# Performance work log

Hardware: AMD Instinct MI355X
Metric: run time of the kernel (lower is better)

## Reference

```python
import jax, jax.numpy as jnp
import numpy as np

HEADS = 8
DIM_HEAD = 64


def setup_inputs() -> dict:
    key = jax.random.key(0)
    ks = jax.random.split(key, 4)
    dim, h, w = 256, 64, 64
    hidden = HEADS * DIM_HEAD  # 512
    return {
        "x": jax.random.normal(ks[0], (dim, h, w), dtype=jnp.float32),
        "gamma": jnp.zeros((dim, 1, 1), dtype=jnp.float32),
        "mem_kv": jax.random.normal(ks[1], (2, HEADS, 4, DIM_HEAD), dtype=jnp.float32),
        "w_qkv": jax.random.normal(ks[2], (3 * hidden, dim), dtype=jnp.float32) * (dim ** -0.5),
        "w_out": jax.random.normal(ks[3], (dim, hidden), dtype=jnp.float32) * (hidden ** -0.5),
    }


def reference(x, gamma, mem_kv, w_qkv, w_out):
    c, h, w = x.shape
    scale = DIM_HEAD ** -0.5
    # RMSNorm over channel axis (axis 0), computed in fp32 like precision_cast
    xf = x.astype(jnp.float32)
    xn = (xf / jnp.linalg.norm(xf, ord=2, axis=0) * (gamma + 1.0) * (c ** 0.5)).astype(x.dtype)
    # 1x1 conv == channel matmul: (3*hidden, c) @ (c, h*w)
    qkv = jnp.einsum('oc,chw->ohw', w_qkv, xn)
    q, k, v = jnp.split(qkv, 3, axis=0)
    # '(h c) x y -> h (x y) c' with heads outermost in the channel dim
    def to_tokens(t):
        return t.reshape(HEADS, DIM_HEAD, h * w).transpose(0, 2, 1)  # [H, S, D]
    q, k, v = map(to_tokens, (q, k, v))
    k = jnp.concatenate([mem_kv[0], k], axis=-2)  # [H, M+S, D]
    v = jnp.concatenate([mem_kv[1], v], axis=-2)
    sim = jnp.einsum('hid,hjd->hij', q * scale, k)  # [H, S, M+S]
    # softmax(sim - global_max) in fp32 == stable softmax along last axis
    attn = jax.nn.softmax((sim - jnp.max(sim)).astype(jnp.float32), axis=-1).astype(sim.dtype)
    out = jnp.einsum('hij,hjd->hid', attn, v)  # [H, S, D]
    # 'h (x y) d -> (h d) x y'
    out = out.reshape(HEADS, h, w, DIM_HEAD).transpose(0, 3, 1, 2).reshape(HEADS * DIM_HEAD, h, w)
    return jnp.einsum('oc,chw->ohw', w_out, out)
```

## Files before the change

kernel.cpp:

```cpp
#include <hip/hip_runtime.h>
#include <hip/hip_bf16.h>
#include <math.h>

#define C_DIM 256
#define SPAT 4096
#define HEADS_N 8
#define DHEAD 64
#define MEMTOK 4
#define TTOK 4100
#define TTOKP 4160
#define HID 512
#define PSP 72

typedef __bf16 bf16x8 __attribute__((ext_vector_type(8)));
typedef unsigned short u16x8 __attribute__((ext_vector_type(8)));
typedef float f32x4 __attribute__((ext_vector_type(4)));

static __device__ inline unsigned short f2bf(float f) {
    unsigned int u = __float_as_uint(f);
    u += 0x7fffu + ((u >> 16) & 1u);
    return (unsigned short)(u >> 16);
}

static __device__ inline bf16x8 ldb8(const unsigned short* p) {
    union { u16x8 u; bf16x8 b; } t;
    t.u = *(const u16x8*)p;
    return t.b;
}

static __device__ inline unsigned int pkbf(float a, float b) {
    union { __bf16 h[2]; unsigned int u; } t;
    t.h[0] = (__bf16)a; t.h[1] = (__bf16)b;
    return t.u;
}

static __device__ inline void gload16(const void* g, void* l) {
    __builtin_amdgcn_global_load_lds(
        (const __attribute__((address_space(1))) unsigned int*)g,
        (__attribute__((address_space(3))) unsigned int*)l, 16, 0, 0);
}

__global__ __launch_bounds__(256) void prep_kernel(
    const float* __restrict__ x, const float* __restrict__ gamma,
    const float* __restrict__ mem, const float* __restrict__ wq,
    const float* __restrict__ wo,
    unsigned short* __restrict__ xb, float* __restrict__ spb,
    unsigned short* __restrict__ wb, unsigned short* __restrict__ wob,
    unsigned short* __restrict__ kb, unsigned short* __restrict__ vtb) {
    __shared__ float XT[64][65];
    __shared__ float red[4][64];
    const int bid = blockIdx.x;
    const int t = threadIdx.x;
    if (bid < 256) {
        int p0 = (bid & 63) * 64, c0 = (bid >> 6) * 64;
#pragma unroll
        for (int i = 0; i < 4; ++i) {
            int cl = i * 16 + (t >> 4), p4 = (t & 15) * 4;
            *(float4*)&XT[cl][p4] = *(const float4*)&x[(size_t)(c0 + cl) * SPAT + p0 + p4];
        }
        __syncthreads();
        int pl = t >> 2, cs = (t & 3) * 16;
        u16x8 a, b;
#pragma unroll
        for (int j = 0; j < 8; ++j) a[j] = f2bf(XT[cs + j][pl]);
#pragma unroll
        for (int j = 0; j < 8; ++j) b[j] = f2bf(XT[cs + 8 + j][pl]);
        *(u16x8*)&xb[(size_t)(p0 + pl) * C_DIM + c0 + cs] = a;
        *(u16x8*)&xb[(size_t)(p0 + pl) * C_DIM + c0 + cs + 8] = b;
    } else if (bid < 320) {
        int p = (bid - 256) * 64 + (t & 63);
        int g = t >> 6;
        float ss = 0.f;
        for (int c = g * 64; c < g * 64 + 64; ++c) {
            float v = x[(size_t)c * SPAT + p];
            ss += v * v;
        }
        red[g][t & 63] = ss;
        __syncthreads();
        if (g == 0) {
            int lp = t & 63;
            float tot = red[0][lp] + red[1][lp] + red[2][lp] + red[3][lp];
            spb[p] = rsqrtf(tot) * 16.0f;
        }
    } else if (bid < 512) {
        size_t idx = ((size_t)(bid - 320) * 256 + t) * 8;
        int c0 = (int)(idx & 255);
        float4 f0 = *(const float4*)&wq[idx];
        float4 f1 = *(const float4*)&wq[idx + 4];
        float4 g0 = *(const float4*)&gamma[c0];
        float4 g1 = *(const float4*)&gamma[c0 + 4];
        u16x8 pk;
        pk[0] = f2bf(f0.x * (g0.x + 1.f)); pk[1] = f2bf(f0.y * (g0.y + 1.f));
        pk[2] = f2bf(f0.z * (g0.z + 1.f)); pk[3] = f2bf(f0.w * (g0.w + 1.f));
        pk[4] = f2bf(f1.x * (g1.x + 1.f)); pk[5] = f2bf(f1.y * (g1.y + 1.f));
        pk[6] = f2bf(f1.z * (g1.z + 1.f)); pk[7] = f2bf(f1.w * (g1.w + 1.f));
        *(u16x8*)&wb[idx] = pk;
    } else if (bid < 576) {
        size_t idx = ((size_t)(bid - 512) * 256 + t) * 8;
        float4 f0 = *(const float4*)&wo[idx];
        float4 f1 = *(const float4*)&wo[idx + 4];
        u16x8 pk;
        pk[0] = f2bf(f0.x); pk[1] = f2bf(f0.y); pk[2] = f2bf(f0.z); pk[3] = f2bf(f0.w);
        pk[4] = f2bf(f1.x); pk[5] = f2bf(f1.y); pk[6] = f2bf(f1.z); pk[7] = f2bf(f1.w);
        *(u16x8*)&wob[idx] = pk;
    } else {
        int i = (bid - 576) * 256 + t;
        if (i < 4096) {
            int d = i & 63, m = (i >> 6) & 3, h = (i >> 8) & 7, s = (i >> 11) & 1;
            unsigned short val = f2bf(mem[i]);
            if (s == 0) kb[(size_t)h * TTOKP * 64 + m * 64 + d] = val;
            else        vtb[((size_t)h * 64 + d) * TTOKP + m] = val;
        } else {
            int z = i - 4096;
            if (z < 30720) {
                int h = z / 3840, r = z % 3840;
                int row = TTOK + r / 64, d = r % 64;
                kb[(size_t)h * TTOKP * 64 + row * 64 + d] = 0;
            } else {
                z -= 30720;
                int h = z / 3840, r = z % 3840;
                int d = r / 60, tcol = TTOK + r % 60;
                vtb[((size_t)h * 64 + d) * TTOKP + tcol] = 0;
            }
        }
    }
}

__global__ __launch_bounds__(256) void qkv_mfma(const unsigned short* __restrict__ wb,
                                                const unsigned short* __restrict__ xb,
                                                const float* __restrict__ spb,
                                                unsigned short* __restrict__ qb,
                                                unsigned short* __restrict__ kb,
                                                unsigned short* __restrict__ vtb) {
    const int tile_p = blockIdx.x;
    const int tile_o = blockIdx.y;
    const int p0 = tile_p * 64, o0 = tile_o * 64;
    __shared__ unsigned short SW[64 * 256];
    __shared__ unsigned short SX[64 * 256];

    const int t = threadIdx.x;
    const int w = t >> 6, lane = t & 63;
    const int col16 = lane & 15, quad = lane >> 4;

    {
        const char* gw = (const char*)(wb + (size_t)o0 * C_DIM);
        const char* gx = (const char*)(xb + (size_t)p0 * C_DIM);
#pragma unroll
        for (int i = 0; i < 8; ++i) {
            int chunk = i * 4 + w;
            int row = chunk * 2 + (lane >> 5);
            int b = (lane & 31) * 16;
            int src = row * 512 + (b ^ ((row & 7) << 4));
            gload16(gw + src, (char*)SW + chunk * 1024);
            gload16(gx + src, (char*)SX + chunk * 1024);
        }
    }
    asm volatile("s_waitcnt vmcnt(0)\n\ts_barrier" ::: "memory");
    __builtin_amdgcn_sched_barrier(0);

    const int cs = (col16 & 7) << 4;
    const char* swp = (const char*)SW;
    const char* sxp = (const char*)SX;
    const int arow = (w * 16 + col16) * 512;
    f32x4 acc[4];
#pragma unroll
    for (int n = 0; n < 4; ++n) acc[n] = (f32x4){0.f, 0.f, 0.f, 0.f};
#pragma unroll
    for (int kk = 0; kk < 8; ++kk) {
        int ko = (kk * 64 + quad * 16) ^ cs;
        bf16x8 a = ldb8((const unsigned short*)(swp + arow + ko));
#pragma unroll
        for (int n = 0; n < 4; ++n) {
            bf16x8 b = ldb8((const unsigned short*)(sxp + (n * 16 + col16) * 512 + ko));
            acc[n] = __builtin_amdgcn_mfma_f32_16x16x32_bf16(a, b, acc[n], 0, 0, 0);
        }
    }

    float spv[4];
#pragma unroll
    for (int n = 0; n < 4; ++n) spv[n] = spb[p0 + n * 16 + col16];

    const int sec = tile_o >> 3, h = tile_o & 7;
    if (sec < 2) {
        const float qsc = (sec == 0) ? 0.125f * 1.4426950408889634f : 1.0f;
        unsigned short* Ot = SW;
        __syncthreads();
#pragma unroll
        for (int n = 0; n < 4; ++n) {
            float s = qsc * spv[n];
            ushort4 v4 = {f2bf(acc[n][0] * s), f2bf(acc[n][1] * s),
                          f2bf(acc[n][2] * s), f2bf(acc[n][3] * s)};
            *(ushort4*)&Ot[(n * 16 + col16) * PSP + w * 16 + quad * 4] = v4;
        }
        __syncthreads();
        int prow = t >> 2, dseg = t & 3;
        u16x8 va = *(u16x8*)&Ot[prow * PSP + dseg * 16];
        u16x8 vb = *(u16x8*)&Ot[prow * PSP + dseg * 16 + 8];
        unsigned short* dst = (sec == 0)
            ? qb + (size_t)h * SPAT * 64 + (size_t)(p0 + prow) * 64
            : kb + (size_t)h * TTOKP * 64 + (size_t)(MEMTOK + p0 + prow) * 64;
        *(u16x8*)&dst[dseg * 16] = va;
        *(u16x8*)&dst[dseg * 16 + 8] = vb;
    } else {
        unsigned short* dst = vtb + (size_t)h * 64 * TTOKP;
#pragma unroll
        for (int n = 0; n < 4; ++n) {
            int tcol = MEMTOK + p0 + n * 16 + col16;
            float s = spv[n];
#pragma unroll
            for (int r = 0; r < 4; ++r)
                dst[(size_t)(w * 16 + quad * 4 + r) * TTOKP + tcol] = f2bf(acc[n][r] * s);
        }
    }
}

__global__ __launch_bounds__(256) void attn_mfma(const unsigned short* __restrict__ qb,
                                                 const unsigned short* __restrict__ kb,
                                                 const unsigned short* __restrict__ vtb,
                                                 unsigned short* __restrict__ obb) {
    const int h  = blockIdx.x & 7;
    const int p0 = (blockIdx.x >> 3) * 64;

    __shared__ unsigned short Ks0[64 * 64], Ks1[64 * 64];
    __shared__ unsigned short Vs0[64 * 64], Vs1[64 * 64];
    __shared__ __bf16 Psb[4 * 16 * PSP];

    const int t = threadIdx.x;
    const int w = t >> 6;
    const int lane = t & 63;
    const int col16 = lane & 15;
    const int quad = lane >> 4;

    const unsigned short* qh = qb + (size_t)h * SPAT * 64;
    const char* khb = (const char*)(kb + (size_t)h * TTOKP * 64);
    const char* vhb = (const char*)(vtb + (size_t)h * 64 * TTOKP);

    const int srow = w * 16 + (lane >> 3);
    const int scol = (((lane & 7) ^ ((lane >> 3) & 7)) << 4);

    const int cswz = col16 & 7;
    const int sw0 = ((quad ^ cswz) << 4);
    const int sw1 = (((quad + 4) ^ cswz) << 4);
    const int rB = col16 * 128;

    bf16x8 aq0 = ldb8(&qh[(size_t)(p0 + w * 16 + col16) * 64 + quad * 8]);
    bf16x8 aq1 = ldb8(&qh[(size_t)(p0 + w * 16 + col16) * 64 + 32 + quad * 8]);

    float m_i = -1e30f, l_i = 0.f;
    f32x4 Oa[4];
#pragma unroll
    for (int n = 0; n < 4; ++n) Oa[n] = (f32x4){0.f, 0.f, 0.f, 0.f};

    __bf16* pw = &Psb[(w * 16 + col16) * PSP];
    const unsigned short* pr = (const unsigned short*)pw;

    auto STAGE = [&](int tb, unsigned short* Kd, unsigned short* Vd) {
        size_t kro = ((size_t)tb * 64 + srow) * 128 + scol;
        gload16(khb + kro,        (char*)Kd + w * 2048);
        gload16(khb + kro + 1024, (char*)Kd + w * 2048 + 1024);
        size_t vro = (size_t)srow * (TTOKP * 2) + (size_t)tb * 128 + scol;
        gload16(vhb + vro,                           (char*)Vd + w * 2048);
        gload16(vhb + vro + (size_t)8 * (TTOKP * 2), (char*)Vd + w * 2048 + 1024);
    };

    auto STEP = [&](int tile, const unsigned short* Kc_, const unsigned short* Vc_,
                    unsigned short* Ksn, unsigned short* Vsn, bool stage, bool last) {
        if (stage) STAGE(tile + 1, Ksn, Vsn);

        const char* Kc = (const char*)Kc_;
        const char* Vc = (const char*)Vc_;

        f32x4 sv[4];
#pragma unroll
        for (int n = 0; n < 4; ++n) {
            sv[n] = (f32x4){0.f, 0.f, 0.f, 0.f};
            bf16x8 bk0 = ldb8((const unsigned short*)(Kc + n * 2048 + rB + sw0));
            bf16x8 bk1 = ldb8((const unsigned short*)(Kc + n * 2048 + rB + sw1));
            sv[n] = __builtin_amdgcn_mfma_f32_16x16x32_bf16(bk0, aq0, sv[n], 0, 0, 0);
            sv[n] = __builtin_amdgcn_mfma_f32_16x16x32_bf16(bk1, aq1, sv[n], 0, 0, 0);
        }

        if (last) {
#pragma unroll
            for (int n = 0; n < 4; ++n)
#pragma unroll
                for (int r = 0; r < 4; ++r)
                    if ((n | quad) != 0) sv[n][r] = -1e30f;
        }

        float rm = fmaxf(
            fmaxf(fmaxf(fmaxf(sv[0][0], sv[0][1]), fmaxf(sv[0][2], sv[0][3])),
                  fmaxf(fmaxf(sv[1][0], sv[1][1]), fmaxf(sv[1][2], sv[1][3]))),
            fmaxf(fmaxf(fmaxf(sv[2][0], sv[2][1]), fmaxf(sv[2][2], sv[2][3])),
                  fmaxf(fmaxf(sv[3][0], sv[3][1]), fmaxf(sv[3][2], sv[3][3]))));
        rm = fmaxf(rm, __shfl_xor(rm, 16, 64));
        rm = fmaxf(rm, __shfl_xor(rm, 32, 64));

        float mn = fmaxf(m_i, rm);
        float al = __builtin_amdgcn_exp2f(m_i - mn);
        m_i = mn;

        float rs = 0.f;
#pragma unroll
        for (int n = 0; n < 4; ++n) {
            float e0 = __builtin_amdgcn_exp2f(sv[n][0] - mn);
            float e1 = __builtin_amdgcn_exp2f(sv[n][1] - mn);
            float e2 = __builtin_amdgcn_exp2f(sv[n][2] - mn);
            float e3 = __builtin_amdgcn_exp2f(sv[n][3] - mn);
            rs += (e0 + e1) + (e2 + e3);
            *(unsigned int*)&pw[n * 16 + quad * 4]     = pkbf(e0, e1);
            *(unsigned int*)&pw[n * 16 + quad * 4 + 2] = pkbf(e2, e3);
        }
        rs += __shfl_xor(rs, 16, 64);
        rs += __shfl_xor(rs, 32, 64);
        l_i = l_i * al + rs;

#pragma unroll
        for (int n = 0; n < 4; ++n) {
            Oa[n][0] *= al; Oa[n][1] *= al; Oa[n][2] *= al; Oa[n][3] *= al;
        }

        bf16x8 pa0 = ldb8(pr + quad * 8);
        bf16x8 pa1 = ldb8(pr + 32 + quad * 8);

#pragma unroll
        for (int n = 0; n < 4; ++n) {
            bf16x8 bv0 = ldb8((const unsigned short*)(Vc + n * 2048 + rB + sw0));
            bf16x8 bv1 = ldb8((const unsigned short*)(Vc + n * 2048 + rB + sw1));
            Oa[n] = __builtin_amdgcn_mfma_f32_16x16x32_bf16(bv0, pa0, Oa[n], 0, 0, 0);
            Oa[n] = __builtin_amdgcn_mfma_f32_16x16x32_bf16(bv1, pa1, Oa[n], 0, 0, 0);
        }

        if (!last) {
            asm volatile("s_waitcnt vmcnt(0)\n\ts_barrier" ::: "memory");
            __builtin_amdgcn_sched_barrier(0);
        }
    };

    STAGE(0, Ks0, Vs0);
    asm volatile("s_waitcnt vmcnt(0)\n\ts_barrier" ::: "memory");
    __builtin_amdgcn_sched_barrier(0);

    for (int b = 0; b < 64; b += 2) {
        STEP(b,     Ks0, Vs0, Ks1, Vs1, true, false);
        STEP(b + 1, Ks1, Vs1, Ks0, Vs0, true, false);
    }
    STEP(64, Ks0, Vs0, Ks1, Vs1, false, true);

    float inv = 1.0f / l_i;
    __bf16* ot = &Psb[(size_t)w * 16 * PSP];
#pragma unroll
    for (int n = 0; n < 4; ++n) {
        *(unsigned int*)&ot[col16 * PSP + n * 16 + quad * 4] =
            pkbf(Oa[n][0] * inv, Oa[n][1] * inv);
        *(unsigned int*)&ot[col16 * PSP + n * 16 + quad * 4 + 2] =
            pkbf(Oa[n][2] * inv, Oa[n][3] * inv);
    }
    int q2 = lane >> 2, dseg = (lane & 3) * 16;
    const unsigned short* otr = (const unsigned short*)ot;
    u16x8 o0v = *(const u16x8*)&otr[q2 * PSP + dseg];
    u16x8 o1v = *(const u16x8*)&otr[q2 * PSP + dseg + 8];
    unsigned short* dst = obb + (size_t)(p0 + w * 16 + q2) * HID + h * DHEAD + dseg;
    *(u16x8*)&dst[0] = o0v;
    *(u16x8*)&dst[8] = o1v;
}

__global__ __launch_bounds__(256) void out_mfma(const unsigned short* __restrict__ wob,
                                                const unsigned short* __restrict__ obb,
                                                float* __restrict__ out) {
    const int p0 = blockIdx.x * 64;
    const int o0 = blockIdx.y * 64;
    __shared__ unsigned short SW[64 * 256];
    __shared__ unsigned short SO[64 * 256];
    __shared__ float OT[4][16 * 68];

    const int t = threadIdx.x;
    const int w = t >> 6, lane = t & 63;
    const int col16 = lane & 15, quad = lane >> 4;
    const int cs = (col16 & 7) << 4;
    const int arow = (w * 16 + col16) * 512;

    f32x4 acc[4];
#pragma unroll
    for (int n = 0; n < 4; ++n) acc[n] = (f32x4){0.f, 0.f, 0.f, 0.f};

#pragma unroll
    for (int ks = 0; ks < 2; ++ks) {
        const char* gw = (const char*)(wob + (size_t)o0 * HID) + ks * 512;
        const char* go = (const char*)(obb + (size_t)p0 * HID) + ks * 512;
#pragma unroll
        for (int i = 0; i < 8; ++i) {
            int chunk = i * 4 + w;
            int row = chunk * 2 + (lane >> 5);
            int b = (lane & 31) * 16;
            int src = row * 1024 + (b ^ ((row & 7) << 4));
            gload16(gw + src, (char*)SW + chunk * 1024);
            gload16(go + src, (char*)SO + chunk * 1024);
        }
        asm volatile("s_waitcnt vmcnt(0)\n\ts_barrier" ::: "memory");
        __builtin_amdgcn_sched_barrier(0);
        const char* swp = (const char*)SW;
        const char* sop = (const char*)SO;
#pragma unroll
        for (int kk = 0; kk < 8; ++kk) {
            int ko = (kk * 64 + quad * 16) ^ cs;
            bf16x8 a = ldb8((const unsigned short*)(swp + arow + ko));
#pragma unroll
            for (int n = 0; n < 4; ++n) {
                bf16x8 bfr = ldb8((const unsigned short*)(sop + (n * 16 + col16) * 512 + ko));
                acc[n] = __builtin_amdgcn_mfma_f32_16x16x32_bf16(a, bfr, acc[n], 0, 0, 0);
            }
        }
        if (ks == 0) __syncthreads();
    }

    float* otw = OT[w];
#pragma unroll
    for (int n = 0; n < 4; ++n)
#pragma unroll
        for (int r = 0; r < 4; ++r)
            otw[(quad * 4 + r) * 68 + n * 16 + col16] = acc[n][r];
    int r2 = lane >> 2, csg = (lane & 3) * 16;
#pragma unroll
    for (int j = 0; j < 4; ++j) {
        float4 v = *(const float4*)&otw[r2 * 68 + csg + j * 4];
        *(float4*)&out[(size_t)(o0 + w * 16 + r2) * SPAT + p0 + csg + j * 4] = v;
    }
}

extern "C" void kernel_launch(void* const* d_in, const int* in_sizes, int n_in,
                              void* d_out, int out_size, void* d_ws, size_t ws_size,
                              hipStream_t stream) {
    const float* x      = (const float*)d_in[0];
    const float* gamma  = (const float*)d_in[1];
    const float* mem_kv = (const float*)d_in[2];
    const float* w_qkv  = (const float*)d_in[3];
    const float* w_out  = (const float*)d_in[4];
    float* out = (float*)d_out;

    unsigned short* xb  = (unsigned short*)d_ws;
    unsigned short* wb  = xb + (size_t)SPAT * C_DIM;
    unsigned short* wob = wb + (size_t)3 * HID * C_DIM;
    unsigned short* qb  = wob + (size_t)C_DIM * HID;
    unsigned short* kb  = qb + (size_t)HEADS_N * SPAT * DHEAD;
    unsigned short* vtb = kb + (size_t)HEADS_N * TTOKP * DHEAD;
    unsigned short* obb = vtb + (size_t)HEADS_N * DHEAD * TTOKP;
    float* spb = (float*)(obb + (size_t)SPAT * HID);

    prep_kernel<<<dim3(832), 256, 0, stream>>>(x, gamma, mem_kv, w_qkv, w_out,
                                               xb, spb, wb, wob, kb, vtb);
    qkv_mfma<<<dim3(64, 24), 256, 0, stream>>>(wb, xb, spb, qb, kb, vtb);
    attn_mfma<<<dim3(512), 256, 0, stream>>>(qb, kb, vtb, obb);
    out_mfma<<<dim3(64, 4), 256, 0, stream>>>(wob, obb, out);
}
```

Measured before the change: 167.0 us.

## Double-buffer GEMM stages and widen attention key tiles with register-held probabilities

The attention kernel now processes 128 keys per step instead of 64. It keeps the softmax probabilities in registers as the MFMA B operand, which removes the LDS round trip, and it permutes the V layout so the packed probabilities line up. The QKV and output projection kernels split the K dimension into 128-wide chunks and double-buffer them, so global-to-LDS loads overlap MFMA compute. The token padding grows to 4224 to fit the larger tiles. This adds register pressure and more masked padding work on the last tile.

```diff
diff --git a/kernel.cpp b/kernel.cpp
--- a/kernel.cpp
+++ b/kernel.cpp
@@ -8,7 +8,7 @@
 #define DHEAD 64
 #define MEMTOK 4
 #define TTOK 4100
-#define TTOKP 4160
+#define TTOKP 4224
 #define HID 512
 #define PSP 72
 
@@ -22,7 +22,7 @@
     return (unsigned short)(u >> 16);
 }
 
-static __device__ inline bf16x8 ldb8(const unsigned short* p) {
+static __device__ inline bf16x8 ldb8(const void* p) {
     union { u16x8 u; bf16x8 b; } t;
     t.u = *(const u16x8*)p;
     return t.b;
@@ -34,11 +34,19 @@
     return t.u;
 }
 
+static __device__ inline int pinv(int m) {
+    return (m & 3) | (((m >> 4) & 1) << 2) | (((m >> 2) & 3) << 3);
+}
+
 static __device__ inline void gload16(const void* g, void* l) {
     __builtin_amdgcn_global_load_lds(
         (const __attribute__((address_space(1))) unsigned int*)g,
         (__attribute__((address_space(3))) unsigned int*)l, 16, 0, 0);
 }
+
+#define DRAIN_BAR() do { \
+    asm volatile("s_waitcnt vmcnt(0)\n\ts_barrier" ::: "memory"); \
+    __builtin_amdgcn_sched_barrier(0); } while (0)
 
 __global__ __launch_bounds__(256) void prep_kernel(
     const float* __restrict__ x, const float* __restrict__ gamma,
@@ -112,14 +120,14 @@
             else        vtb[((size_t)h * 64 + d) * TTOKP + m] = val;
         } else {
             int z = i - 4096;
-            if (z < 30720) {
-                int h = z / 3840, r = z % 3840;
+            if (z < 63488) {
+                int h = z / 7936, r = z % 7936;
                 int row = TTOK + r / 64, d = r % 64;
                 kb[(size_t)h * TTOKP * 64 + row * 64 + d] = 0;
             } else {
-                z -= 30720;
-                int h = z / 3840, r = z % 3840;
-                int d = r / 60, tcol = TTOK + r % 60;
+                z -= 63488;
+                int h = z / 7936, r = z % 7936;
+                int d = r / 124, tcol = TTOK + r % 124;
                 vtb[((size_t)h * 64 + d) * TTOKP + tcol] = 0;
             }
         }
@@ -135,46 +143,51 @@
     const int tile_p = blockIdx.x;
     const int tile_o = blockIdx.y;
     const int p0 = tile_p * 64, o0 = tile_o * 64;
-    __shared__ unsigned short SW[64 * 256];
-    __shared__ unsigned short SX[64 * 256];
+    __shared__ unsigned short LB[4][64 * 128];
 
     const int t = threadIdx.x;
     const int w = t >> 6, lane = t & 63;
     const int col16 = lane & 15, quad = lane >> 4;
-
-    {
-        const char* gw = (const char*)(wb + (size_t)o0 * C_DIM);
-        const char* gx = (const char*)(xb + (size_t)p0 * C_DIM);
-#pragma unroll
-        for (int i = 0; i < 8; ++i) {
-            int chunk = i * 4 + w;
-            int row = chunk * 2 + (lane >> 5);
-            int b = (lane & 31) * 16;
-            int src = row * 512 + (b ^ ((row & 7) << 4));
-            gload16(gw + src, (char*)SW + chunk * 1024);
-            gload16(gx + src, (char*)SX + chunk * 1024);
-        }
-    }
-    asm volatile("s_waitcnt vmcnt(0)\n\ts_barrier" ::: "memory");
-    __builtin_amdgcn_sched_barrier(0);
-
-    const int cs = (col16 & 7) << 4;
-    const char* swp = (const char*)SW;
-    const char* sxp = (const char*)SX;
-    const int arow = (w * 16 + col16) * 512;
+    const int c7 = col16 & 7;
+    const char* gw = (const char*)(wb + (size_t)o0 * C_DIM);
+    const char* gx = (const char*)(xb + (size_t)p0 * C_DIM);
+
+    auto STG = [&](int ck, unsigned short* SWb, unsigned short* SXb) {
+#pragma unroll
+        for (int i = 0; i < 4; ++i) {
+            int c4 = w * 4 + i;
+            int row = c4 * 4 + (lane >> 4);
+            int sl = (((lane & 15) ^ (row & 7)) << 4);
+            size_t src = (size_t)row * 512 + ck * 256 + sl;
+            gload16(gw + src, (char*)SWb + c4 * 1024);
+            gload16(gx + src, (char*)SXb + c4 * 1024);
+        }
+    };
+
     f32x4 acc[4];
 #pragma unroll
     for (int n = 0; n < 4; ++n) acc[n] = (f32x4){0.f, 0.f, 0.f, 0.f};
-#pragma unroll
-    for (int kk = 0; kk < 8; ++kk) {
-        int ko = (kk * 64 + quad * 16) ^ cs;
-        bf16x8 a = ldb8((const unsigned short*)(swp + arow + ko));
-#pragma unroll
-        for (int n = 0; n < 4; ++n) {
-            bf16x8 b = ldb8((const unsigned short*)(sxp + (n * 16 + col16) * 512 + ko));
-            acc[n] = __builtin_amdgcn_mfma_f32_16x16x32_bf16(a, b, acc[n], 0, 0, 0);
-        }
-    }
+    const int arow = (w * 16 + col16) * 256;
+
+    auto COMP = [&](const unsigned short* SWb, const unsigned short* SXb) {
+#pragma unroll
+        for (int kkl = 0; kkl < 4; ++kkl) {
+            int ko = (((kkl * 4 + quad) ^ c7) << 4);
+            bf16x8 a = ldb8((const char*)SWb + arow + ko);
+#pragma unroll
+            for (int n = 0; n < 4; ++n) {
+                bf16x8 b = ldb8((const char*)SXb + (n * 16 + col16) * 256 + ko);
+                acc[n] = __builtin_amdgcn_mfma_f32_16x16x32_bf16(a, b, acc[n], 0, 0, 0);
+            }
+        }
+    };
+
+    STG(0, LB[0], LB[1]);
+    DRAIN_BAR();
+    STG(1, LB[2], LB[3]);
+    COMP(LB[0], LB[1]);
+    DRAIN_BAR();
+    COMP(LB[2], LB[3]);
 
     float spv[4];
 #pragma unroll
@@ -183,7 +196,7 @@
     const int sec = tile_o >> 3, h = tile_o & 7;
     if (sec < 2) {
         const float qsc = (sec == 0) ? 0.125f * 1.4426950408889634f : 1.0f;
-        unsigned short* Ot = SW;
+        unsigned short* Ot = &LB[0][0];
         __syncthreads();
 #pragma unroll
         for (int n = 0; n < 4; ++n) {
@@ -205,11 +218,12 @@
         unsigned short* dst = vtb + (size_t)h * 64 * TTOKP;
 #pragma unroll
         for (int n = 0; n < 4; ++n) {
-            int tcol = MEMTOK + p0 + n * 16 + col16;
+            int tg = MEMTOK + p0 + n * 16 + col16;
+            int c = (tg & ~31) | pinv(tg & 31);
             float s = spv[n];
 #pragma unroll
             for (int r = 0; r < 4; ++r)
-                dst[(size_t)(w * 16 + quad * 4 + r) * TTOKP + tcol] = f2bf(acc[n][r] * s);
+                dst[(size_t)(w * 16 + quad * 4 + r) * TTOKP + c] = f2bf(acc[n][r] * s);
         }
     }
 }
@@ -221,28 +235,21 @@
     const int h  = blockIdx.x & 7;
     const int p0 = (blockIdx.x >> 3) * 64;
 
-    __shared__ unsigned short Ks0[64 * 64], Ks1[64 * 64];
-    __shared__ unsigned short Vs0[64 * 64], Vs1[64 * 64];
-    __shared__ __bf16 Psb[4 * 16 * PSP];
+    __shared__ unsigned short LA[4][64 * 128];
 
     const int t = threadIdx.x;
     const int w = t >> 6;
     const int lane = t & 63;
     const int col16 = lane & 15;
     const int quad = lane >> 4;
+    const int cswz = col16 & 7;
+    const int sw0 = ((quad ^ cswz) << 4);
+    const int sw1 = (((quad + 4) ^ cswz) << 4);
 
     const unsigned short* qh = qb + (size_t)h * SPAT * 64;
     const char* khb = (const char*)(kb + (size_t)h * TTOKP * 64);
     const char* vhb = (const char*)(vtb + (size_t)h * 64 * TTOKP);
 
-    const int srow = w * 16 + (lane >> 3);
-    const int scol = (((lane & 7) ^ ((lane >> 3) & 7)) << 4);
-
-    const int cswz = col16 & 7;
-    const int sw0 = ((quad ^ cswz) << 4);
-    const int sw1 = (((quad + 4) ^ cswz) << 4);
-    const int rB = col16 * 128;
-
     bf16x8 aq0 = ldb8(&qh[(size_t)(p0 + w * 16 + col16) * 64 + quad * 8]);
     bf16x8 aq1 = ldb8(&qh[(size_t)(p0 + w * 16 + col16) * 64 + 32 + quad * 8]);
 
@@ -251,16 +258,18 @@
 #pragma unroll
     for (int n = 0; n < 4; ++n) Oa[n] = (f32x4){0.f, 0.f, 0.f, 0.f};
 
-    __bf16* pw = &Psb[(w * 16 + col16) * PSP];
-    const unsigned short* pr = (const unsigned short*)pw;
-
     auto STAGE = [&](int tb, unsigned short* Kd, unsigned short* Vd) {
-        size_t kro = ((size_t)tb * 64 + srow) * 128 + scol;
-        gload16(khb + kro,        (char*)Kd + w * 2048);
-        gload16(khb + kro + 1024, (char*)Kd + w * 2048 + 1024);
-        size_t vro = (size_t)srow * (TTOKP * 2) + (size_t)tb * 128 + scol;
-        gload16(vhb + vro,                           (char*)Vd + w * 2048);
-        gload16(vhb + vro + (size_t)8 * (TTOKP * 2), (char*)Vd + w * 2048 + 1024);
+#pragma unroll
+        for (int i = 0; i < 4; ++i) {
+            int ck = w * 4 + i;
+            int krow = ck * 8 + (lane >> 3);
+            int kcol = (((lane & 7) ^ (lane >> 3)) << 4);
+            gload16(khb + (size_t)(tb * 128 + krow) * 128 + kcol, (char*)Kd + ck * 1024);
+            int vrow = ck * 4 + (lane >> 4);
+            int vcol = (((lane & 15) ^ (vrow & 7)) << 4);
+            gload16(vhb + (size_t)vrow * (TTOKP * 2) + (size_t)tb * 256 + vcol,
+                    (char*)Vd + ck * 1024);
+        }
     };
 
     auto STEP = [&](int tile, const unsigned short* Kc_, const unsigned short* Vc_,
@@ -270,29 +279,30 @@
         const char* Kc = (const char*)Kc_;
         const char* Vc = (const char*)Vc_;
 
-        f32x4 sv[4];
-#pragma unroll
-        for (int n = 0; n < 4; ++n) {
+        f32x4 sv[8];
+#pragma unroll
+        for (int n = 0; n < 8; ++n) {
             sv[n] = (f32x4){0.f, 0.f, 0.f, 0.f};
-            bf16x8 bk0 = ldb8((const unsigned short*)(Kc + n * 2048 + rB + sw0));
-            bf16x8 bk1 = ldb8((const unsigned short*)(Kc + n * 2048 + rB + sw1));
+            bf16x8 bk0 = ldb8(Kc + (n * 16 + col16) * 128 + sw0);
+            bf16x8 bk1 = ldb8(Kc + (n * 16 + col16) * 128 + sw1);
             sv[n] = __builtin_amdgcn_mfma_f32_16x16x32_bf16(bk0, aq0, sv[n], 0, 0, 0);
             sv[n] = __builtin_amdgcn_mfma_f32_16x16x32_bf16(bk1, aq1, sv[n], 0, 0, 0);
         }
 
         if (last) {
 #pragma unroll
-            for (int n = 0; n < 4; ++n)
+            for (int n = 0; n < 8; ++n)
 #pragma unroll
                 for (int r = 0; r < 4; ++r)
                     if ((n | quad) != 0) sv[n][r] = -1e30f;
         }
 
-        float rm = fmaxf(
-            fmaxf(fmaxf(fmaxf(sv[0][0], sv[0][1]), fmaxf(sv[0][2], sv[0][3])),
-                  fmaxf(fmaxf(sv[1][0], sv[1][1]), fmaxf(sv[1][2], sv[1][3]))),
-            fmaxf(fmaxf(fmaxf(sv[2][0], sv[2][1]), fmaxf(sv[2][2], sv[2][3])),
-                  fmaxf(fmaxf(sv[3][0], sv[3][1]), fmaxf(sv[3][2], sv[3][3]))));
+        float mx[8];
+#pragma unroll
+        for (int n = 0; n < 8; ++n)
+            mx[n] = fmaxf(fmaxf(sv[n][0], sv[n][1]), fmaxf(sv[n][2], sv[n][3]));
+        float rm = fmaxf(fmaxf(fmaxf(mx[0], mx[1]), fmaxf(mx[2], mx[3])),
+                         fmaxf(fmaxf(mx[4], mx[5]), fmaxf(mx[6], mx[7])));
         rm = fmaxf(rm, __shfl_xor(rm, 16, 64));
         rm = fmaxf(rm, __shfl_xor(rm, 32, 64));
 
@@ -300,17 +310,18 @@
         float al = __builtin_amdgcn_exp2f(m_i - mn);
         m_i = mn;
 
-        float rs = 0.f;
-#pragma unroll
-        for (int n = 0; n < 4; ++n) {
+        float sm[8];
+#pragma unroll
+        for (int n = 0; n < 8; ++n) {
             float e0 = __builtin_amdgcn_exp2f(sv[n][0] - mn);
             float e1 = __builtin_amdgcn_exp2f(sv[n][1] - mn);
             float e2 = __builtin_amdgcn_exp2f(sv[n][2] - mn);
             float e3 = __builtin_amdgcn_exp2f(sv[n][3] - mn);
-            rs += (e0 + e1) + (e2 + e3);
-            *(unsigned int*)&pw[n * 16 + quad * 4]     = pkbf(e0, e1);
-            *(unsigned int*)&pw[n * 16 + quad * 4 + 2] = pkbf(e2, e3);
-        }
+            sv[n][0] = e0; sv[n][1] = e1; sv[n][2] = e2; sv[n][3] = e3;
+            sm[n] = (e0 + e1) + (e2 + e3);
+        }
+        float rs = ((sm[0] + sm[1]) + (sm[2] + sm[3])) +
+                   ((sm[4] + sm[5]) + (sm[6] + sm[7]));
         rs += __shfl_xor(rs, 16, 64);
         rs += __shfl_xor(rs, 32, 64);
         l_i = l_i * al + rs;
@@ -320,35 +331,35 @@
             Oa[n][0] *= al; Oa[n][1] *= al; Oa[n][2] *= al; Oa[n][3] *= al;
         }
 
-        bf16x8 pa0 = ldb8(pr + quad * 8);
-        bf16x8 pa1 = ldb8(pr + 32 + quad * 8);
-
-#pragma unroll
-        for (int n = 0; n < 4; ++n) {
-            bf16x8 bv0 = ldb8((const unsigned short*)(Vc + n * 2048 + rB + sw0));
-            bf16x8 bv1 = ldb8((const unsigned short*)(Vc + n * 2048 + rB + sw1));
-            Oa[n] = __builtin_amdgcn_mfma_f32_16x16x32_bf16(bv0, pa0, Oa[n], 0, 0, 0);
-            Oa[n] = __builtin_amdgcn_mfma_f32_16x16x32_bf16(bv1, pa1, Oa[n], 0, 0, 0);
-        }
-
-        if (!last) {
-            asm volatile("s_waitcnt vmcnt(0)\n\ts_barrier" ::: "memory");
-            __builtin_amdgcn_sched_barrier(0);
-        }
-    };
-
-    STAGE(0, Ks0, Vs0);
-    asm volatile("s_waitcnt vmcnt(0)\n\ts_barrier" ::: "memory");
-    __builtin_amdgcn_sched_barrier(0);
-
-    for (int b = 0; b < 64; b += 2) {
-        STEP(b,     Ks0, Vs0, Ks1, Vs1, true, false);
-        STEP(b + 1, Ks1, Vs1, Ks0, Vs0, true, false);
+#pragma unroll
+        for (int f = 0; f < 4; ++f) {
+            union { unsigned int u[4]; bf16x8 v; } pu;
+            pu.u[0] = pkbf(sv[2 * f][0], sv[2 * f][1]);
+            pu.u[1] = pkbf(sv[2 * f][2], sv[2 * f][3]);
+            pu.u[2] = pkbf(sv[2 * f + 1][0], sv[2 * f + 1][1]);
+            pu.u[3] = pkbf(sv[2 * f + 1][2], sv[2 * f + 1][3]);
+            int vo = (((f * 4 + quad) ^ cswz) << 4);
+#pragma unroll
+            for (int n = 0; n < 4; ++n) {
+                bf16x8 bv = ldb8(Vc + (n * 16 + col16) * 256 + vo);
+                Oa[n] = __builtin_amdgcn_mfma_f32_16x16x32_bf16(bv, pu.v, Oa[n], 0, 0, 0);
+            }
+        }
+
+        if (!last) DRAIN_BAR();
+    };
+
+    STAGE(0, LA[0], LA[1]);
+    DRAIN_BAR();
+    for (int b = 0; b < 32; b += 2) {
+        STEP(b,     LA[0], LA[1], LA[2], LA[3], true, false);
+        STEP(b + 1, LA[2], LA[3], LA[0], LA[1], true, false);
     }
-    STEP(64, Ks0, Vs0, Ks1, Vs1, false, true);
-
+    STEP(32, LA[0], LA[1], LA[2], LA[3], false, true);
+
+    __syncthreads();
     float inv = 1.0f / l_i;
-    __bf16* ot = &Psb[(size_t)w * 16 * PSP];
+    __bf16* ot = (__bf16*)&LA[0][0] + (size_t)w * 16 * PSP;
 #pragma unroll
     for (int n = 0; n < 4; ++n) {
         *(unsigned int*)&ot[col16 * PSP + n * 16 + quad * 4] =
@@ -370,51 +381,54 @@
                                                 float* __restrict__ out) {
     const int p0 = blockIdx.x * 64;
     const int o0 = blockIdx.y * 64;
-    __shared__ unsigned short SW[64 * 256];
-    __shared__ unsigned short SO[64 * 256];
-    __shared__ float OT[4][16 * 68];
+    __shared__ unsigned short LB[4][64 * 128];
 
     const int t = threadIdx.x;
     const int w = t >> 6, lane = t & 63;
     const int col16 = lane & 15, quad = lane >> 4;
-    const int cs = (col16 & 7) << 4;
-    const int arow = (w * 16 + col16) * 512;
+    const int c7 = col16 & 7;
+    const char* gw = (const char*)(wob + (size_t)o0 * HID);
+    const char* go = (const char*)(obb + (size_t)p0 * HID);
+
+    auto STG = [&](int ck, unsigned short* SWb, unsigned short* SOb) {
+#pragma unroll
+        for (int i = 0; i < 4; ++i) {
+            int c4 = w * 4 + i;
+            int row = c4 * 4 + (lane >> 4);
+            int sl = (((lane & 15) ^ (row & 7)) << 4);
+            size_t src = (size_t)row * 1024 + ck * 256 + sl;
+            gload16(gw + src, (char*)SWb + c4 * 1024);
+            gload16(go + src, (char*)SOb + c4 * 1024);
+        }
+    };
 
     f32x4 acc[4];
 #pragma unroll
     for (int n = 0; n < 4; ++n) acc[n] = (f32x4){0.f, 0.f, 0.f, 0.f};
-
-#pragma unroll
-    for (int ks = 0; ks < 2; ++ks) {
-        const char* gw = (const char*)(wob + (size_t)o0 * HID) + ks * 512;
-        const char* go = (const char*)(obb + (size_t)p0 * HID) + ks * 512;
-#pragma unroll
-        for (int i = 0; i < 8; ++i) {
-            int chunk = i * 4 + w;
-            int row = chunk * 2 + (lane >> 5);
-            int b = (lane & 31) * 16;
-            int src = row * 1024 + (b ^ ((row & 7) << 4));
-            gload16(gw + src, (char*)SW + chunk * 1024);
-            gload16(go + src, (char*)SO + chunk * 1024);
-        }
-        asm volatile("s_waitcnt vmcnt(0)\n\ts_barrier" ::: "memory");
-        __builtin_amdgcn_sched_barrier(0);
-        const char* swp = (const char*)SW;
-        const char* sop = (const char*)SO;
-#pragma unroll
-        for (int kk = 0; kk < 8; ++kk) {
-            int ko = (kk * 64 + quad * 16) ^ cs;
-            bf16x8 a = ldb8((const unsigned short*)(swp + arow + ko));
+    const int arow = (w * 16 + col16) * 256;
+
+    auto COMP = [&](const unsigned short* SWb, const unsigned short* SOb) {
+#pragma unroll
+        for (int kkl = 0; kkl < 4; ++kkl) {
+            int ko = (((kkl * 4 + quad) ^ c7) << 4);
+            bf16x8 a = ldb8((const char*)SWb + arow + ko);
 #pragma unroll
             for (int n = 0; n < 4; ++n) {
-                bf16x8 bfr = ldb8((const unsigned short*)(sop + (n * 16 + col16) * 512 + ko));
-                acc[n] = __builtin_amdgcn_mfma_f32_16x16x32_bf16(a, bfr, acc[n], 0, 0, 0);
+                bf16x8 b = ldb8((const char*)SOb + (n * 16 + col16) * 256 + ko);
+                acc[n] = __builtin_amdgcn_mfma_f32_16x16x32_bf16(a, b, acc[n], 0, 0, 0);
             }
         }
-        if (ks == 0) __syncthreads();
-    }
-
-    float* otw = OT[w];
+    };
+
+    STG(0, LB[0], LB[1]);
+    DRAIN_BAR();
+    STG(1, LB[2], LB[3]);  COMP(LB[0], LB[1]);  DRAIN_BAR();
+    STG(2, LB[0], LB[1]);  COMP(LB[2], LB[3]);  DRAIN_BAR();
+    STG(3, LB[2], LB[3]);  COMP(LB[0], LB[1]);  DRAIN_BAR();
+    COMP(LB[2], LB[3]);
+
+    __syncthreads();
+    float* otw = (float*)&LB[0][0] + (size_t)w * (16 * 68);
 #pragma unroll
     for (int n = 0; n < 4; ++n)
 #pragma unroll
@@ -447,8 +461,8 @@
     unsigned short* obb = vtb + (size_t)HEADS_N * DHEAD * TTOKP;
     float* spb = (float*)(obb + (size_t)SPAT * HID);
 
-    prep_kernel<<<dim3(832), 256, 0, stream>>>(x, gamma, mem_kv, w_qkv, w_out,
-                                               xb, spb, wb, wob, kb, vtb);
+    prep_kernel<<<dim3(1088), 256, 0, stream>>>(x, gamma, mem_kv, w_qkv, w_out,
+                                                xb, spb, wb, wob, kb, vtb);
     qkv_mfma<<<dim3(64, 24), 256, 0, stream>>>(wb, xb, spb, qb, kb, vtb);
     attn_mfma<<<dim3(512), 256, 0, stream>>>(qb, kb, vtb, obb);
     out_mfma<<<dim3(64, 4), 256, 0, stream>>>(wob, obb, out);
```

New measurement: 156.9 us. -6.0%, faster.
